# Kernel tuning notes

Hardware: AMD Instinct MI355X
Metric: run time of the kernel (lower is better)

Reference implementation:

```python
import jax, jax.numpy as jnp
import numpy as np

HEADS = 20
SHIFT = 0.6931471805599453  # style_alignment_score_shift = log(2)
KEY_SCALE = 1.0             # style_alignment_score_scale
EPS = 1e-5


def expand_first(feat, scale=1.0):
    # feat: [B, H, S, D]; broadcast style features (batch items 0 and B//2)
    b = feat.shape[0]
    fs = jnp.stack([feat[0], feat[b // 2]])[:, None]           # [2,1,H,S,D]
    fs = jnp.broadcast_to(fs, (2, b // 2) + feat.shape[1:])    # [2,B/2,H,S,D]
    if scale != 1:
        fs = jnp.concatenate([fs[:, :1], scale * fs[:, 1:]], axis=1)
    return fs.reshape(feat.shape)


def concat_first(feat, scale=1.0):
    # concatenate style features along the sequence axis (-2)
    return jnp.concatenate([feat, expand_first(feat, scale=scale)], axis=-2)


def adain(feat):
    # stats over sequence axis (-2); torch .var() is unbiased (ddof=1)
    mean = feat.mean(axis=-2, keepdims=True)
    std = jnp.sqrt(feat.var(axis=-2, keepdims=True, ddof=1) + EPS)
    sm = expand_first(mean)
    ss = expand_first(std)
    return (feat - mean) / std * ss + sm


def setup_inputs() -> dict:
    key = jax.random.key(0)
    ks = jax.random.split(key, 6)
    B, S, C = 4, 1024, 1280
    sc = 1.0 / np.sqrt(C)
    return {
        "hidden_states": jax.random.normal(ks[0], (B, S, C), jnp.float32),
        "Wq": jax.random.normal(ks[1], (C, C), jnp.float32) * sc,
        "Wk": jax.random.normal(ks[2], (C, C), jnp.float32) * sc,
        "Wv": jax.random.normal(ks[3], (C, C), jnp.float32) * sc,
        "Wo": jax.random.normal(ks[4], (C, C), jnp.float32) * sc,
        "bo": jnp.zeros((C,), jnp.float32),
    }


def reference(hidden_states, Wq, Wk, Wv, Wo, bo):
    B, S, C = hidden_states.shape
    H = HEADS
    hd = C // H
    scale = hd ** -0.5

    def to_heads(t):  # [B,S,C] -> [B,H,S,hd]
        return t.reshape(B, S, H, hd).transpose(0, 2, 1, 3)

    q = to_heads(hidden_states @ Wq.T)
    k = to_heads(hidden_states @ Wk.T)
    v = to_heads(hidden_states @ Wv.T)

    q = adain(q)              # adain_queries
    k = adain(k)              # adain_keys
    # adain_values = False

    k = concat_first(k, scale=KEY_SCALE)   # [B,H,2S,hd]
    v = concat_first(v)                    # [B,H,2S,hd]

    # shifted scaled dot-product attention (shift added to shared-key block)
    logits = jnp.einsum('bhqd,bhkd->bhqk', q, k) * scale  # [B,H,S,2S]
    bias = jnp.where(jnp.arange(k.shape[-2]) >= S, jnp.float32(SHIFT), jnp.float32(0.0))
    probs = jax.nn.softmax(logits + bias, axis=-1)
    out = jnp.einsum('bhqk,bhkd->bhqd', probs, v)         # [B,H,S,hd]

    out = out.transpose(0, 2, 1, 3).reshape(B, S, C)
    out = out @ Wo.T + bo
    return out
```

## Files before the change

### kernel.cpp

```cpp
#include <hip/hip_runtime.h>
#include <math.h>


typedef __bf16 bf16x8 __attribute__((ext_vector_type(8)));
typedef __bf16 bf16x2_t __attribute__((ext_vector_type(2)));
typedef float f32x4 __attribute__((ext_vector_type(4)));
typedef unsigned short u16x8 __attribute__((ext_vector_type(8)));

#define BDIM 256

__device__ inline unsigned short f2bf(float f) {
  return __builtin_bit_cast(unsigned short, (__bf16)f);
}
__device__ inline unsigned int pack_bf2(float lo, float hi) {
  bf16x2_t v;
  v[0] = (__bf16)lo;
  v[1] = (__bf16)hi;
  return __builtin_bit_cast(unsigned int, v);
}
__device__ inline float bf2f(unsigned short h) {
  return __uint_as_float(((unsigned int)h) << 16);
}

__device__ inline void gl_lds16(const unsigned short* g, unsigned short* l) {
  __builtin_amdgcn_global_load_lds(
      (const __attribute__((address_space(1))) unsigned int*)g,
      (__attribute__((address_space(3))) unsigned int*)l, 16, 0, 0);
}

__global__ __launch_bounds__(BDIM) void k_convert_all(
    const float* __restrict__ X, const float* __restrict__ Wq,
    const float* __restrict__ Wk, const float* __restrict__ Wv,
    const float* __restrict__ Wo, unsigned short* __restrict__ Xbf,
    unsigned short* __restrict__ Wcat, unsigned short* __restrict__ Wobf) {
  const int idx = blockIdx.x * BDIM + threadIdx.x;
  const float* src;
  unsigned short* dst;
  int off;
  if (idx < 1310720) {
    src = X; dst = Xbf; off = idx;
  } else {
    const int r = idx - 1310720;
    const int which = r / 409600;
    off = r - which * 409600;
    src = (which == 0) ? Wq : (which == 1) ? Wk : (which == 2) ? Wv : Wo;
    dst = (which < 3) ? Wcat + (size_t)which * 1638400 : Wobf;
  }
  const float4 v = ((const float4*)src)[off];
  ushort4 o;
  o.x = f2bf(v.x); o.y = f2bf(v.y); o.z = f2bf(v.z); o.w = f2bf(v.w);
  ((ushort4*)dst)[off] = o;
}

__global__ __launch_bounds__(512, 1) void k_gemm_bf16(
    const unsigned short* __restrict__ A, const unsigned short* __restrict__ B,
    unsigned short* __restrict__ Cbf, int M, int N, int K) {
  __shared__ unsigned short lds[2][2][16384];

  const int bid = blockIdx.x;
  const int swz = (bid & 7) * 30 + (bid >> 3);
  const int mt = swz & 15, nt = swz >> 4;
  const int mBase = mt * 256, nBase = nt * 256;

  const int t = threadIdx.x;
  const int w = t >> 6, lane = t & 63, quad = lane >> 4, l16 = lane & 15;
  const int wrow = w & 1, wcol = w >> 1;
  const int glg = (lane & 7) ^ ((lane >> 3) & 7);
  const int NTILES = K >> 6;

  f32x4 acc[8][4];
#pragma unroll
  for (int i = 0; i < 8; ++i)
#pragma unroll
    for (int j = 0; j < 4; ++j) acc[i][j] = (f32x4){0.f, 0.f, 0.f, 0.f};

  auto stage = [&](int s, int kt) {
#pragma unroll
    for (int j = 0; j < 4; ++j) {
      const int row = j * 64 + w * 8 + (lane >> 3);
      gl_lds16(A + (size_t)(mBase + row) * K + kt * 64 + glg * 8,
               &lds[s][0][(j * 512 + w * 64 + lane) * 8]);
    }
#pragma unroll
    for (int j = 0; j < 4; ++j) {
      const int row = j * 64 + w * 8 + (lane >> 3);
      gl_lds16(B + (size_t)(nBase + row) * K + kt * 64 + glg * 8,
               &lds[s][1][(j * 512 + w * 64 + lane) * 8]);
    }
  };

  stage(0, 0);
  stage(1, 1);
  asm volatile("s_waitcnt vmcnt(8)" ::: "memory");
  __builtin_amdgcn_s_barrier();

  const int arow0 = (wrow * 128 + l16) * 64;
  const int brow0 = (wcol * 64 + l16) * 64;
  const int g0 = ((quad) ^ (l16 & 7)) * 8;
  const int g1 = ((4 + quad) ^ (l16 & 7)) * 8;

  for (int kt = 0; kt < NTILES; ++kt) {
    const int s = kt & 1;
    if (kt >= 1 && kt + 1 < NTILES) stage(s ^ 1, kt + 1);
    const unsigned short* As = &lds[s][0][0];
    const unsigned short* Bs = &lds[s][1][0];
#pragma unroll
    for (int ph = 0; ph < 4; ++ph) {
      const int mh = ph >> 1, nh = ph & 1;
      bf16x8 af[4][2], bq[2][2];
#pragma unroll
      for (int mi = 0; mi < 4; ++mi) {
        const int ro = arow0 + (mh * 4 + mi) * 1024;
        af[mi][0] = *(const bf16x8*)(As + ro + g0);
        af[mi][1] = *(const bf16x8*)(As + ro + g1);
      }
#pragma unroll
      for (int ni = 0; ni < 2; ++ni) {
        const int ro = brow0 + (nh * 2 + ni) * 1024;
        bq[ni][0] = *(const bf16x8*)(Bs + ro + g0);
        bq[ni][1] = *(const bf16x8*)(Bs + ro + g1);
      }
      __builtin_amdgcn_s_setprio(1);
#pragma unroll
      for (int kk = 0; kk < 2; ++kk)
#pragma unroll
        for (int mi = 0; mi < 4; ++mi)
#pragma unroll
          for (int ni = 0; ni < 2; ++ni)
            acc[mh * 4 + mi][nh * 2 + ni] =
                __builtin_amdgcn_mfma_f32_16x16x32_bf16(
                    af[mi][kk], bq[ni][kk], acc[mh * 4 + mi][nh * 2 + ni], 0,
                    0, 0);
      __builtin_amdgcn_s_setprio(0);
      if (ph < 3) __builtin_amdgcn_s_barrier();
    }
    asm volatile("s_waitcnt vmcnt(0)" ::: "memory");
    __builtin_amdgcn_s_barrier();
  }

#pragma unroll
  for (int mi = 0; mi < 8; ++mi)
#pragma unroll
    for (int r = 0; r < 4; ++r) {
      const int row = mBase + wrow * 128 + mi * 16 + quad * 4 + r;
#pragma unroll
      for (int ni = 0; ni < 4; ++ni)
        Cbf[(size_t)row * N + nBase + wcol * 64 + ni * 16 + l16] =
            f2bf(acc[mi][ni][r]);
    }
}

__global__ __launch_bounds__(BDIM, 2) void k_gemm_out(
    const unsigned short* __restrict__ A, const unsigned short* __restrict__ B,
    float* __restrict__ Cf, const float* __restrict__ bias, int M, int N,
    int K) {
  __shared__ unsigned short lds[2][2][8192];

  const int bid = blockIdx.x;
  const int swz = (bid & 7) * 40 + (bid >> 3);
  const int mt = swz & 31, nt = swz >> 5;
  const int mBase = mt * 128, nBase = nt * 128;

  const int t = threadIdx.x;
  const int w = t >> 6, lane = t & 63, quad = lane >> 4, l16 = lane & 15;
  const int wrow = w & 1, wcol = w >> 1;
  const int glg = (lane & 7) ^ ((lane >> 3) & 7);
  const int NTILES = K >> 6;

  f32x4 acc[4][4];
#pragma unroll
  for (int i = 0; i < 4; ++i)
#pragma unroll
    for (int j = 0; j < 4; ++j) acc[i][j] = (f32x4){0.f, 0.f, 0.f, 0.f};

  auto stage = [&](int s, int kt) {
#pragma unroll
    for (int j = 0; j < 4; ++j) {
      const int row = j * 32 + (t >> 3);
      gl_lds16(A + (size_t)(mBase + row) * K + kt * 64 + glg * 8,
               &lds[s][0][(j * 256 + t) * 8]);
    }
#pragma unroll
    for (int j = 0; j < 4; ++j) {
      const int row = j * 32 + (t >> 3);
      gl_lds16(B + (size_t)(nBase + row) * K + kt * 64 + glg * 8,
               &lds[s][1][(j * 256 + t) * 8]);
    }
  };

  stage(0, 0);
  stage(1, 1);
  asm volatile("s_waitcnt vmcnt(8)" ::: "memory");
  __builtin_amdgcn_s_barrier();

  const int arow0 = (wrow * 64 + l16) * 64;
  const int brow0 = (wcol * 64 + l16) * 64;
  const int g0 = ((quad) ^ (l16 & 7)) * 8;
  const int g1 = ((4 + quad) ^ (l16 & 7)) * 8;

  for (int kt = 0; kt < NTILES; ++kt) {
    const int s = kt & 1;
    if (kt >= 1 && kt + 1 < NTILES) stage(s ^ 1, kt + 1);
    const unsigned short* As = &lds[s][0][0];
    const unsigned short* Bs = &lds[s][1][0];
#pragma unroll
    for (int ph = 0; ph < 2; ++ph) {
      bf16x8 af[2][2], bq[4][2];
#pragma unroll
      for (int mi = 0; mi < 2; ++mi) {
        const int ro = arow0 + (ph * 2 + mi) * 1024;
        af[mi][0] = *(const bf16x8*)(As + ro + g0);
        af[mi][1] = *(const bf16x8*)(As + ro + g1);
      }
#pragma unroll
      for (int ni = 0; ni < 4; ++ni) {
        const int ro = brow0 + ni * 1024;
        bq[ni][0] = *(const bf16x8*)(Bs + ro + g0);
        bq[ni][1] = *(const bf16x8*)(Bs + ro + g1);
      }
      __builtin_amdgcn_s_setprio(1);
#pragma unroll
      for (int kk = 0; kk < 2; ++kk)
#pragma unroll
        for (int mi = 0; mi < 2; ++mi)
#pragma unroll
          for (int ni = 0; ni < 4; ++ni)
            acc[ph * 2 + mi][ni] = __builtin_amdgcn_mfma_f32_16x16x32_bf16(
                af[mi][kk], bq[ni][kk], acc[ph * 2 + mi][ni], 0, 0, 0);
      __builtin_amdgcn_s_setprio(0);
      if (ph == 0) __builtin_amdgcn_s_barrier();
    }
    asm volatile("s_waitcnt vmcnt(0)" ::: "memory");
    __builtin_amdgcn_s_barrier();
  }

#pragma unroll
  for (int mi = 0; mi < 4; ++mi)
#pragma unroll
    for (int r = 0; r < 4; ++r) {
      const int row = mBase + wrow * 64 + mi * 16 + quad * 4 + r;
#pragma unroll
      for (int ni = 0; ni < 4; ++ni) {
        const int col = nBase + wcol * 64 + ni * 16 + l16;
        Cf[(size_t)row * N + col] = acc[mi][ni][r] + bias[col];
      }
    }
}

__global__ __launch_bounds__(320) void k_stats1(
    const unsigned short* __restrict__ QKV, float* __restrict__ psum,
    float* __restrict__ psq) {
  const int z = blockIdx.y, which = z >> 2, b = z & 3;
  const int c = threadIdx.x * 4;
  const size_t base =
      (size_t)(b * 1024 + blockIdx.x * 32) * 3840 + which * 1280 + c;
  float4 s = {0.f, 0.f, 0.f, 0.f}, s2 = {0.f, 0.f, 0.f, 0.f};
#pragma unroll 8
  for (int i = 0; i < 32; ++i) {
    const ushort4 xv = *(const ushort4*)(QKV + base + (size_t)i * 3840);
    const float x0 = bf2f(xv.x), x1 = bf2f(xv.y), x2 = bf2f(xv.z),
                x3 = bf2f(xv.w);
    s.x += x0; s.y += x1; s.z += x2; s.w += x3;
    s2.x = fmaf(x0, x0, s2.x); s2.y = fmaf(x1, x1, s2.y);
    s2.z = fmaf(x2, x2, s2.z); s2.w = fmaf(x3, x3, s2.w);
  }
  const size_t o = ((size_t)z * 32 + blockIdx.x) * 1280 + c;
  *(float4*)(psum + o) = s;
  *(float4*)(psq + o) = s2;
}

__global__ __launch_bounds__(BDIM) void k_stats2(
    const float* __restrict__ psum, const float* __restrict__ psq,
    float* __restrict__ stats) {
  const int z = blockIdx.y, which = z >> 2, b = z & 3;
  const int c = blockIdx.x * 256 + threadIdx.x;
  float s = 0.f, s2 = 0.f;
#pragma unroll
  for (int j = 0; j < 32; ++j) {
    s += psum[((size_t)z * 32 + j) * 1280 + c];
    s2 += psq[((size_t)z * 32 + j) * 1280 + c];
  }
  const float mean = s * (1.0f / 1024.0f);
  const float var = (s2 - 1024.0f * mean * mean) * (1.0f / 1023.0f);
  stats[((which * 2 + 0) * 4 + b) * 1280 + c] = mean;
  stats[((which * 2 + 1) * 4 + b) * 1280 + c] = sqrtf(var + 1e-5f);
}

__global__ __launch_bounds__(BDIM) void k_adain_vt(
    const unsigned short* __restrict__ QKV, const float* __restrict__ stats,
    unsigned short* __restrict__ qn, unsigned short* __restrict__ kn,
    unsigned short* __restrict__ vt) {
  __shared__ unsigned short tile[64][65];
  const int bx = blockIdx.x;
  if (bx < 10240) {
    const int which = bx / 5120;
    const int rem = bx - which * 5120;
    const int b = rem / 1280;
    const int xb = rem - b * 1280;
    const int idx = xb * BDIM + threadIdx.x;
    const int s = idx / 320;
    const int c = (idx - s * 320) * 4;
    const int sb = (b < 2) ? 0 : 2;
    const ushort4 xv = *(const ushort4*)(QKV + ((size_t)(b * 1024 + s)) * 3840 +
                                         which * 1280 + c);
    const float4 mean =
        *(const float4*)(stats + ((which * 2 + 0) * 4 + b) * 1280 + c);
    const float4 stdv =
        *(const float4*)(stats + ((which * 2 + 1) * 4 + b) * 1280 + c);
    const float4 meanS =
        *(const float4*)(stats + ((which * 2 + 0) * 4 + sb) * 1280 + c);
    const float4 stdS =
        *(const float4*)(stats + ((which * 2 + 1) * 4 + sb) * 1280 + c);
    ushort4 o;
    o.x = f2bf((bf2f(xv.x) - mean.x) / stdv.x * stdS.x + meanS.x);
    o.y = f2bf((bf2f(xv.y) - mean.y) / stdv.y * stdS.y + meanS.y);
    o.z = f2bf((bf2f(xv.z) - mean.z) / stdv.z * stdS.z + meanS.z);
    o.w = f2bf((bf2f(xv.w) - mean.w) / stdv.w * stdS.w + meanS.w);
    unsigned short* dst = (which == 0) ? qn : kn;
    *(ushort4*)(dst + ((size_t)(b * 1024 + s)) * 1280 + c) = o;
  } else {
    const int tb = bx - 10240;
    const int b = tb / 320;
    const int r2 = tb - b * 320;
    const int c0 = (r2 / 16) * 64;
    const int s0 = (r2 & 15) * 64;
    const int t = threadIdx.x;
    const int r = t >> 2, seg = (t & 3) * 16;
    const size_t goff = ((size_t)(b * 1024 + s0 + r)) * 3840 + 2560 + c0 + seg;
    const u16x8 va = *(const u16x8*)(QKV + goff);
    const u16x8 vb = *(const u16x8*)(QKV + goff + 8);
#pragma unroll
    for (int j = 0; j < 8; j++) {
      tile[r][seg + j] = va[j];
      tile[r][seg + 8 + j] = vb[j];
    }
    __syncthreads();
    u16x8 o0, o1;
#pragma unroll
    for (int j = 0; j < 8; j++) {
      o0[j] = tile[seg + j][r];
      o1[j] = tile[seg + 8 + j][r];
    }
    const size_t ooff = ((size_t)(b * 1280 + c0 + r)) * 1024 + s0 + seg;
    *(u16x8*)(vt + ooff) = o0;
    *(u16x8*)(vt + ooff + 8) = o1;
  }
}

__global__ __launch_bounds__(BDIM, 4) void k_attn(
    const unsigned short* __restrict__ qn, const unsigned short* __restrict__ kn,
    const unsigned short* __restrict__ vt, unsigned short* __restrict__ Opart,
    float* __restrict__ Lpart) {
  const int S = 1024, C = 1280;
  const int L = blockIdx.x + 8 * (blockIdx.y + 20 * blockIdx.z);
  const int qt = (L >> 3) & 7;
  const int hz = (L & 7) + ((L >> 6) << 3);
  const int h = hz % 20;
  const int zs = hz / 20;
  int b, chunk;
  if (zs < 2)      { b = 0; chunk = zs; }
  else if (zs < 6) { b = 1; chunk = zs - 2; }
  else if (zs < 8) { b = 2; chunk = zs - 6; }
  else             { b = 3; chunk = zs - 8; }
  const int ktBeg = chunk * 8;
  const int t = threadIdx.x, w = t >> 6, lane = t & 63;
  const int quad = lane >> 4, l16 = lane & 15;
  const int bstyle = (b < 2) ? 0 : 2;
  const int qrow = qt * 128 + w * 32;

  __shared__ unsigned short Ks[2][2][64 * 32];
  __shared__ unsigned short Vs[2][64 * 32];
  __shared__ unsigned short Plds[4][32][64];

  bf16x8 aq[2][2];
#pragma unroll
  for (int g = 0; g < 2; ++g) {
    const size_t qoff =
        ((size_t)(b * S + qrow + g * 16 + l16)) * C + h * 64 + quad * 8;
    aq[g][0] = *(const bf16x8*)(qn + qoff);
    aq[g][1] = *(const bf16x8*)(qn + qoff + 32);
  }

  bf16x8 ones;
#pragma unroll
  for (int i = 0; i < 8; ++i) ones[i] = (__bf16)1.0f;

  f32x4 o[2][4], lsum[2];
#pragma unroll
  for (int g = 0; g < 2; ++g) {
    lsum[g] = (f32x4){0.f, 0.f, 0.f, 0.f};
#pragma unroll
    for (int i = 0; i < 4; i++) o[g][i] = (f32x4){0.f, 0.f, 0.f, 0.f};
  }

  const int krow = t >> 2;
  const int kseg = ((t & 3) ^ ((t >> 3) & 3)) * 8;
  const int sw = l16 & 14;
  const int qsw = (quad ^ ((l16 >> 1) & 3)) * 8;

  auto stageK = [&](int buf, int kt) {
    const int bs = (kt < 16) ? b : bstyle;
    const int sk = (kt & 15) * 64;
    const unsigned short* kg =
        kn + (size_t)(bs * S + sk + krow) * C + h * 64 + kseg;
    gl_lds16(kg, Ks[buf][0] + t * 8);
    gl_lds16(kg + 32, Ks[buf][1] + t * 8);
  };
  auto stageV = [&](int kt) {
    const int bs = (kt < 16) ? b : bstyle;
    const int sk = (kt & 15) * 64;
    const unsigned short* vg =
        vt + (size_t)(bs * C + h * 64 + krow) * S + sk + kseg;
    gl_lds16(vg, Vs[0] + t * 8);
    gl_lds16(vg + 32, Vs[1] + t * 8);
  };

  stageK(0, ktBeg);

  const float SCALE2 = 0.125f * 1.44269504088896341f;

  for (int i = 0; i < 8; ++i) {
    const int kt = ktBeg + i;
    const int buf = i & 1;
    asm volatile("s_waitcnt vmcnt(0)" ::: "memory");
    __builtin_amdgcn_s_barrier();
    stageV(kt);
    if (i + 1 < 8) stageK(buf ^ 1, kt + 1);

    const float bias2 = (kt >= 16) ? 1.0f : 0.0f;

    f32x4 z2[2][4];
#pragma unroll
    for (int nt = 0; nt < 4; ++nt) {
      const bf16x8 bk0 =
          *(const bf16x8*)(Ks[buf][0] + (nt * 16 + l16) * 32 + qsw);
      const bf16x8 bk1 =
          *(const bf16x8*)(Ks[buf][1] + (nt * 16 + l16) * 32 + qsw);
#pragma unroll
      for (int g = 0; g < 2; ++g) {
        f32x4 zz = (f32x4){0.f, 0.f, 0.f, 0.f};
        zz = __builtin_amdgcn_mfma_f32_16x16x32_bf16(bk0, aq[g][0], zz, 0, 0, 0);
        zz = __builtin_amdgcn_mfma_f32_16x16x32_bf16(bk1, aq[g][1], zz, 0, 0, 0);
        z2[g][nt] = zz;
      }
    }

#pragma unroll
    for (int g = 0; g < 2; ++g) {
#pragma unroll
      for (int nt = 0; nt < 4; ++nt) {
        const float e0 = exp2f(fmaf(z2[g][nt][0], SCALE2, bias2));
        const float e1 = exp2f(fmaf(z2[g][nt][1], SCALE2, bias2));
        const float e2 = exp2f(fmaf(z2[g][nt][2], SCALE2, bias2));
        const float e3 = exp2f(fmaf(z2[g][nt][3], SCALE2, bias2));
        uint2 pk;
        pk.x = pack_bf2(e0, e1);
        pk.y = pack_bf2(e2, e3);
        const int phys = (nt * 4 + quad) ^ sw;
        *(uint2*)(&Plds[w][g * 16 + l16][phys * 4]) = pk;
      }
    }

    if (i + 1 < 8)
      asm volatile("s_waitcnt vmcnt(2)" ::: "memory");
    else
      asm volatile("s_waitcnt vmcnt(0)" ::: "memory");
    __builtin_amdgcn_s_barrier();

#pragma unroll
    for (int g = 0; g < 2; ++g) {
      const int a0 = (2 * quad) ^ sw;
      const int a1 = (2 * quad + 8) ^ sw;
      const bf16x8 pa0 = *(const bf16x8*)(&Plds[w][g * 16 + l16][a0 * 4]);
      const bf16x8 pa1 = *(const bf16x8*)(&Plds[w][g * 16 + l16][a1 * 4]);
      lsum[g] = __builtin_amdgcn_mfma_f32_16x16x32_bf16(pa0, ones, lsum[g], 0, 0, 0);
      lsum[g] = __builtin_amdgcn_mfma_f32_16x16x32_bf16(pa1, ones, lsum[g], 0, 0, 0);
#pragma unroll
      for (int dt = 0; dt < 4; ++dt) {
        const bf16x8 vb0 =
            *(const bf16x8*)(Vs[0] + (dt * 16 + l16) * 32 + qsw);
        const bf16x8 vb1 =
            *(const bf16x8*)(Vs[1] + (dt * 16 + l16) * 32 + qsw);
        o[g][dt] =
            __builtin_amdgcn_mfma_f32_16x16x32_bf16(pa0, vb0, o[g][dt], 0, 0, 0);
        o[g][dt] =
            __builtin_amdgcn_mfma_f32_16x16x32_bf16(pa1, vb1, o[g][dt], 0, 0, 0);
      }
    }
  }

  if (l16 == 0) {
#pragma unroll
    for (int g = 0; g < 2; ++g)
#pragma unroll
      for (int r = 0; r < 4; ++r)
        Lpart[((size_t)zs * 20 + h) * 1024 + qrow + g * 16 + quad * 4 + r] =
            lsum[g][r];
  }

  unsigned short* Op = Opart + (size_t)zs * 1024 * 1280;
#pragma unroll
  for (int g = 0; g < 2; ++g)
#pragma unroll
    for (int dt = 0; dt < 4; ++dt)
#pragma unroll
      for (int r = 0; r < 4; ++r)
        Op[(size_t)(qrow + g * 16 + quad * 4 + r) * 1280 + h * 64 + dt * 16 +
           l16] = f2bf(o[g][dt][r]);
}

__global__ __launch_bounds__(BDIM) void k_combine(
    const unsigned short* __restrict__ Opart, const float* __restrict__ Lpart,
    unsigned short* __restrict__ attnb) {
  const int idx = blockIdx.x * BDIM + threadIdx.x;
  const int row = idx / 160;
  const int c = (idx - row * 160) * 8;
  const int b = row >> 10, q = row & 1023, h = c >> 6;
  const int zb = (b >> 1) * 6 + (b & 1) * 2;
  const int ns = 2 + (b & 1) * 2;
  float L = 0.f;
  float acc[8] = {0.f, 0.f, 0.f, 0.f, 0.f, 0.f, 0.f, 0.f};
  for (int s = 0; s < ns; ++s) {
    L += Lpart[((size_t)(zb + s) * 20 + h) * 1024 + q];
    const u16x8 v =
        *(const u16x8*)(Opart + (size_t)(zb + s) * 1310720 + (size_t)q * 1280 + c);
#pragma unroll
    for (int j = 0; j < 8; ++j) acc[j] += bf2f(v[j]);
  }
  const float rl = 1.0f / L;
  u16x8 o8;
#pragma unroll
  for (int j = 0; j < 8; ++j) o8[j] = f2bf(acc[j] * rl);
  *(u16x8*)(attnb + (size_t)row * 1280 + c) = o8;
}

extern "C" void kernel_launch(void* const* d_in, const int* in_sizes, int n_in,
                              void* d_out, int out_size, void* d_ws,
                              size_t ws_size, hipStream_t stream) {
  const float* X = (const float*)d_in[0];
  const float* Wq = (const float*)d_in[1];
  const float* Wk = (const float*)d_in[2];
  const float* Wv = (const float*)d_in[3];
  const float* Wo = (const float*)d_in[4];
  const float* bo = (const float*)d_in[5];
  float* out = (float*)d_out;

  char* ws = (char*)d_ws;
  size_t off = 0;
  auto alloc = [&](size_t bytes) {
    char* p = ws + off;
    off += (bytes + 255) & ~(size_t)255;
    return p;
  };
  unsigned short* Wcat = (unsigned short*)alloc(3840ull * 1280 * 2);
  unsigned short* Xbf = (unsigned short*)alloc(4096ull * 1280 * 2);
  unsigned short* QKV = (unsigned short*)alloc(4096ull * 3840 * 2);
  unsigned short* Wobf = (unsigned short*)alloc(1280ull * 1280 * 2);
  float* stats = (float*)alloc(2ull * 2 * 4 * 1280 * 4);
  unsigned short* qnb = (unsigned short*)alloc(4096ull * 1280 * 2);
  unsigned short* knb = (unsigned short*)alloc(4096ull * 1280 * 2);
  unsigned short* vtb = (unsigned short*)alloc(4096ull * 1280 * 2);
  unsigned short* attnb = (unsigned short*)alloc(4096ull * 1280 * 2);

  unsigned short* Opart = QKV;
  float* Lpart = (float*)Wcat;
  float* psum = (float*)attnb;
  float* psq = (float*)(attnb + 4096ull * 1280 / 2);

  k_convert_all<<<11520, BDIM, 0, stream>>>(X, Wq, Wk, Wv, Wo, Xbf, Wcat, Wobf);
  k_gemm_bf16<<<240, 512, 0, stream>>>(Xbf, Wcat, QKV, 4096, 3840, 1280);
  k_stats1<<<dim3(32, 8), 320, 0, stream>>>(QKV, psum, psq);
  k_stats2<<<dim3(5, 8), BDIM, 0, stream>>>(psum, psq, stats);
  k_adain_vt<<<11520, BDIM, 0, stream>>>(QKV, stats, qnb, knb, vtb);
  k_attn<<<dim3(8, 20, 12), BDIM, 0, stream>>>(qnb, knb, vtb, Opart, Lpart);
  k_combine<<<2560, BDIM, 0, stream>>>(Opart, Lpart, attnb);
  k_gemm_out<<<320, BDIM, 0, stream>>>(attnb, Wobf, out, bo, 4096, 1280, 1280);
}
```

Baseline: 262.2 us.

## Fold key AdaIN into query scaling and per-row bias inside attention

The separate AdaIN pass over Q and K is removed. The attention kernel now normalizes Q in registers from raw QKV and reads un-normalized K directly. The key affine transform (gain and offset) is folded algebraically into the query: the gain multiplies the query, and the offset becomes a per-row additive bias reduced by wave shuffles. For style chunks the key stats are treated as identity, which relies on the style batch's keys mapping onto themselves. This saves a full read/write pass over Q and K, at the cost of extra per-block prologue math and the precision risk of rounding the scaled query to bf16. The partial-output buffers are remapped onto Xbf and qnb, because QKV is still being read during attention.

```diff
diff --git a/kernel.cpp b/kernel.cpp
--- a/kernel.cpp
+++ b/kernel.cpp
@@ -286,72 +286,41 @@
   stats[((which * 2 + 1) * 4 + b) * 1280 + c] = sqrtf(var + 1e-5f);
 }
 
-__global__ __launch_bounds__(BDIM) void k_adain_vt(
-    const unsigned short* __restrict__ QKV, const float* __restrict__ stats,
-    unsigned short* __restrict__ qn, unsigned short* __restrict__ kn,
-    unsigned short* __restrict__ vt) {
+__global__ __launch_bounds__(BDIM) void k_vt(
+    const unsigned short* __restrict__ QKV, unsigned short* __restrict__ vt) {
   __shared__ unsigned short tile[64][65];
-  const int bx = blockIdx.x;
-  if (bx < 10240) {
-    const int which = bx / 5120;
-    const int rem = bx - which * 5120;
-    const int b = rem / 1280;
-    const int xb = rem - b * 1280;
-    const int idx = xb * BDIM + threadIdx.x;
-    const int s = idx / 320;
-    const int c = (idx - s * 320) * 4;
-    const int sb = (b < 2) ? 0 : 2;
-    const ushort4 xv = *(const ushort4*)(QKV + ((size_t)(b * 1024 + s)) * 3840 +
-                                         which * 1280 + c);
-    const float4 mean =
-        *(const float4*)(stats + ((which * 2 + 0) * 4 + b) * 1280 + c);
-    const float4 stdv =
-        *(const float4*)(stats + ((which * 2 + 1) * 4 + b) * 1280 + c);
-    const float4 meanS =
-        *(const float4*)(stats + ((which * 2 + 0) * 4 + sb) * 1280 + c);
-    const float4 stdS =
-        *(const float4*)(stats + ((which * 2 + 1) * 4 + sb) * 1280 + c);
-    ushort4 o;
-    o.x = f2bf((bf2f(xv.x) - mean.x) / stdv.x * stdS.x + meanS.x);
-    o.y = f2bf((bf2f(xv.y) - mean.y) / stdv.y * stdS.y + meanS.y);
-    o.z = f2bf((bf2f(xv.z) - mean.z) / stdv.z * stdS.z + meanS.z);
-    o.w = f2bf((bf2f(xv.w) - mean.w) / stdv.w * stdS.w + meanS.w);
-    unsigned short* dst = (which == 0) ? qn : kn;
-    *(ushort4*)(dst + ((size_t)(b * 1024 + s)) * 1280 + c) = o;
-  } else {
-    const int tb = bx - 10240;
-    const int b = tb / 320;
-    const int r2 = tb - b * 320;
-    const int c0 = (r2 / 16) * 64;
-    const int s0 = (r2 & 15) * 64;
-    const int t = threadIdx.x;
-    const int r = t >> 2, seg = (t & 3) * 16;
-    const size_t goff = ((size_t)(b * 1024 + s0 + r)) * 3840 + 2560 + c0 + seg;
-    const u16x8 va = *(const u16x8*)(QKV + goff);
-    const u16x8 vb = *(const u16x8*)(QKV + goff + 8);
-#pragma unroll
-    for (int j = 0; j < 8; j++) {
-      tile[r][seg + j] = va[j];
-      tile[r][seg + 8 + j] = vb[j];
-    }
-    __syncthreads();
-    u16x8 o0, o1;
-#pragma unroll
-    for (int j = 0; j < 8; j++) {
-      o0[j] = tile[seg + j][r];
-      o1[j] = tile[seg + 8 + j][r];
-    }
-    const size_t ooff = ((size_t)(b * 1280 + c0 + r)) * 1024 + s0 + seg;
-    *(u16x8*)(vt + ooff) = o0;
-    *(u16x8*)(vt + ooff + 8) = o1;
-  }
+  const int tb = blockIdx.x;
+  const int b = tb / 320;
+  const int r2 = tb - b * 320;
+  const int c0 = (r2 / 16) * 64;
+  const int s0 = (r2 & 15) * 64;
+  const int t = threadIdx.x;
+  const int r = t >> 2, seg = (t & 3) * 16;
+  const size_t goff = ((size_t)(b * 1024 + s0 + r)) * 3840 + 2560 + c0 + seg;
+  const u16x8 va = *(const u16x8*)(QKV + goff);
+  const u16x8 vb = *(const u16x8*)(QKV + goff + 8);
+#pragma unroll
+  for (int j = 0; j < 8; j++) {
+    tile[r][seg + j] = va[j];
+    tile[r][seg + 8 + j] = vb[j];
+  }
+  __syncthreads();
+  u16x8 o0, o1;
+#pragma unroll
+  for (int j = 0; j < 8; j++) {
+    o0[j] = tile[seg + j][r];
+    o1[j] = tile[seg + 8 + j][r];
+  }
+  const size_t ooff = ((size_t)(b * 1280 + c0 + r)) * 1024 + s0 + seg;
+  *(u16x8*)(vt + ooff) = o0;
+  *(u16x8*)(vt + ooff + 8) = o1;
 }
 
 __global__ __launch_bounds__(BDIM, 4) void k_attn(
-    const unsigned short* __restrict__ qn, const unsigned short* __restrict__ kn,
-    const unsigned short* __restrict__ vt, unsigned short* __restrict__ Opart,
-    float* __restrict__ Lpart) {
-  const int S = 1024, C = 1280;
+    const unsigned short* __restrict__ qkv, const float* __restrict__ stats,
+    const unsigned short* __restrict__ vt, unsigned short* __restrict__ Op0,
+    unsigned short* __restrict__ Op1, float* __restrict__ Lpart) {
+  const int S = 1024;
   const int L = blockIdx.x + 8 * (blockIdx.y + 20 * blockIdx.z);
   const int qt = (L >> 3) & 7;
   const int hz = (L & 7) + ((L >> 6) << 3);
@@ -367,18 +336,76 @@
   const int quad = lane >> 4, l16 = lane & 15;
   const int bstyle = (b < 2) ? 0 : 2;
   const int qrow = qt * 128 + w * 32;
+  const bool style = (ktBeg >= 16);
 
   __shared__ unsigned short Ks[2][2][64 * 32];
   __shared__ unsigned short Vs[2][64 * 32];
   __shared__ unsigned short Plds[4][32][64];
 
+  const float S2 = 0.125f * 1.44269504088896341f;
+
   bf16x8 aq[2][2];
-#pragma unroll
-  for (int g = 0; g < 2; ++g) {
-    const size_t qoff =
-        ((size_t)(b * S + qrow + g * 16 + l16)) * C + h * 64 + quad * 8;
-    aq[g][0] = *(const bf16x8*)(qn + qoff);
-    aq[g][1] = *(const bf16x8*)(qn + qoff + 32);
+  float biasv[2];
+  {
+    float rq[2] = {0.f, 0.f};
+#pragma unroll
+    for (int hf = 0; hf < 2; ++hf) {
+      const int cc = h * 64 + quad * 8 + hf * 32;
+      float mqb[8], sqb[8], mqs[8], sqs[8];
+      *(float4*)(mqb)     = *(const float4*)(stats + (0 + b) * 1280 + cc);
+      *(float4*)(mqb + 4) = *(const float4*)(stats + (0 + b) * 1280 + cc + 4);
+      *(float4*)(sqb)     = *(const float4*)(stats + (4 + b) * 1280 + cc);
+      *(float4*)(sqb + 4) = *(const float4*)(stats + (4 + b) * 1280 + cc + 4);
+      *(float4*)(mqs)     = *(const float4*)(stats + (0 + bstyle) * 1280 + cc);
+      *(float4*)(mqs + 4) = *(const float4*)(stats + (0 + bstyle) * 1280 + cc + 4);
+      *(float4*)(sqs)     = *(const float4*)(stats + (4 + bstyle) * 1280 + cc);
+      *(float4*)(sqs + 4) = *(const float4*)(stats + (4 + bstyle) * 1280 + cc + 4);
+      float gk[8], ok[8];
+      if (!style) {
+        float mkb[8], skb[8], mks[8], sks[8];
+        *(float4*)(mkb)     = *(const float4*)(stats + (8 + b) * 1280 + cc);
+        *(float4*)(mkb + 4) = *(const float4*)(stats + (8 + b) * 1280 + cc + 4);
+        *(float4*)(skb)     = *(const float4*)(stats + (12 + b) * 1280 + cc);
+        *(float4*)(skb + 4) = *(const float4*)(stats + (12 + b) * 1280 + cc + 4);
+        *(float4*)(mks)     = *(const float4*)(stats + (8 + bstyle) * 1280 + cc);
+        *(float4*)(mks + 4) = *(const float4*)(stats + (8 + bstyle) * 1280 + cc + 4);
+        *(float4*)(sks)     = *(const float4*)(stats + (12 + bstyle) * 1280 + cc);
+        *(float4*)(sks + 4) = *(const float4*)(stats + (12 + bstyle) * 1280 + cc + 4);
+#pragma unroll
+        for (int j = 0; j < 8; ++j) {
+          gk[j] = sks[j] / skb[j];
+          ok[j] = mks[j] - mkb[j] * gk[j];
+        }
+      }
+#pragma unroll
+      for (int g = 0; g < 2; ++g) {
+        const size_t qoff =
+            ((size_t)(b * S + qrow + g * 16 + l16)) * 3840 + cc;
+        const bf16x8 qv = *(const bf16x8*)(qkv + qoff);
+        bf16x8 av;
+#pragma unroll
+        for (int j = 0; j < 8; ++j) {
+          const float q = (float)qv[j];
+          const float qn = (q - mqb[j]) / sqb[j] * sqs[j] + mqs[j];
+          float a;
+          if (!style) {
+            rq[g] = fmaf(qn, ok[j], rq[g]);
+            a = qn * gk[j] * S2;
+          } else {
+            a = qn * S2;
+          }
+          av[j] = (__bf16)a;
+        }
+        aq[g][hf] = av;
+      }
+    }
+#pragma unroll
+    for (int g = 0; g < 2; ++g) {
+      float r = rq[g] * S2;
+      r += __shfl_xor(r, 16, 64);
+      r += __shfl_xor(r, 32, 64);
+      biasv[g] = style ? 1.0f : r;
+    }
   }
 
   bf16x8 ones;
@@ -402,7 +429,7 @@
     const int bs = (kt < 16) ? b : bstyle;
     const int sk = (kt & 15) * 64;
     const unsigned short* kg =
-        kn + (size_t)(bs * S + sk + krow) * C + h * 64 + kseg;
+        qkv + (size_t)(bs * S + sk + krow) * 3840 + 1280 + h * 64 + kseg;
     gl_lds16(kg, Ks[buf][0] + t * 8);
     gl_lds16(kg + 32, Ks[buf][1] + t * 8);
   };
@@ -410,14 +437,12 @@
     const int bs = (kt < 16) ? b : bstyle;
     const int sk = (kt & 15) * 64;
     const unsigned short* vg =
-        vt + (size_t)(bs * C + h * 64 + krow) * S + sk + kseg;
+        vt + (size_t)(bs * 1280 + h * 64 + krow) * S + sk + kseg;
     gl_lds16(vg, Vs[0] + t * 8);
     gl_lds16(vg + 32, Vs[1] + t * 8);
   };
 
   stageK(0, ktBeg);
-
-  const float SCALE2 = 0.125f * 1.44269504088896341f;
 
   for (int i = 0; i < 8; ++i) {
     const int kt = ktBeg + i;
@@ -427,8 +452,6 @@
     stageV(kt);
     if (i + 1 < 8) stageK(buf ^ 1, kt + 1);
 
-    const float bias2 = (kt >= 16) ? 1.0f : 0.0f;
-
     f32x4 z2[2][4];
 #pragma unroll
     for (int nt = 0; nt < 4; ++nt) {
@@ -447,12 +470,13 @@
 
 #pragma unroll
     for (int g = 0; g < 2; ++g) {
+      const float bg = biasv[g];
 #pragma unroll
       for (int nt = 0; nt < 4; ++nt) {
-        const float e0 = exp2f(fmaf(z2[g][nt][0], SCALE2, bias2));
-        const float e1 = exp2f(fmaf(z2[g][nt][1], SCALE2, bias2));
-        const float e2 = exp2f(fmaf(z2[g][nt][2], SCALE2, bias2));
-        const float e3 = exp2f(fmaf(z2[g][nt][3], SCALE2, bias2));
+        const float e0 = exp2f(z2[g][nt][0] + bg);
+        const float e1 = exp2f(z2[g][nt][1] + bg);
+        const float e2 = exp2f(z2[g][nt][2] + bg);
+        const float e3 = exp2f(z2[g][nt][3] + bg);
         uint2 pk;
         pk.x = pack_bf2(e0, e1);
         pk.y = pack_bf2(e2, e3);
@@ -498,7 +522,8 @@
             lsum[g][r];
   }
 
-  unsigned short* Op = Opart + (size_t)zs * 1024 * 1280;
+  unsigned short* Op = (zs < 4) ? Op0 + (size_t)zs * 1310720
+                                : Op1 + (size_t)(zs - 4) * 1310720;
 #pragma unroll
   for (int g = 0; g < 2; ++g)
 #pragma unroll
@@ -510,8 +535,8 @@
 }
 
 __global__ __launch_bounds__(BDIM) void k_combine(
-    const unsigned short* __restrict__ Opart, const float* __restrict__ Lpart,
-    unsigned short* __restrict__ attnb) {
+    const unsigned short* __restrict__ Op0, const unsigned short* __restrict__ Op1,
+    const float* __restrict__ Lpart, unsigned short* __restrict__ attnb) {
   const int idx = blockIdx.x * BDIM + threadIdx.x;
   const int row = idx / 160;
   const int c = (idx - row * 160) * 8;
@@ -521,9 +546,12 @@
   float L = 0.f;
   float acc[8] = {0.f, 0.f, 0.f, 0.f, 0.f, 0.f, 0.f, 0.f};
   for (int s = 0; s < ns; ++s) {
-    L += Lpart[((size_t)(zb + s) * 20 + h) * 1024 + q];
-    const u16x8 v =
-        *(const u16x8*)(Opart + (size_t)(zb + s) * 1310720 + (size_t)q * 1280 + c);
+    const int z = zb + s;
+    const unsigned short* base = (z < 4)
+        ? Op0 + (size_t)z * 1310720
+        : Op1 + (size_t)(z - 4) * 1310720;
+    L += Lpart[((size_t)z * 20 + h) * 1024 + q];
+    const u16x8 v = *(const u16x8*)(base + (size_t)q * 1280 + c);
 #pragma unroll
     for (int j = 0; j < 8; ++j) acc[j] += bf2f(v[j]);
   }
@@ -561,8 +589,10 @@
   unsigned short* knb = (unsigned short*)alloc(4096ull * 1280 * 2);
   unsigned short* vtb = (unsigned short*)alloc(4096ull * 1280 * 2);
   unsigned short* attnb = (unsigned short*)alloc(4096ull * 1280 * 2);
-
-  unsigned short* Opart = QKV;
+  (void)knb;
+
+  unsigned short* Op0 = Xbf;
+  unsigned short* Op1 = qnb;
   float* Lpart = (float*)Wcat;
   float* psum = (float*)attnb;
   float* psq = (float*)(attnb + 4096ull * 1280 / 2);
@@ -571,8 +601,9 @@
   k_gemm_bf16<<<240, 512, 0, stream>>>(Xbf, Wcat, QKV, 4096, 3840, 1280);
   k_stats1<<<dim3(32, 8), 320, 0, stream>>>(QKV, psum, psq);
   k_stats2<<<dim3(5, 8), BDIM, 0, stream>>>(psum, psq, stats);
-  k_adain_vt<<<11520, BDIM, 0, stream>>>(QKV, stats, qnb, knb, vtb);
-  k_attn<<<dim3(8, 20, 12), BDIM, 0, stream>>>(qnb, knb, vtb, Opart, Lpart);
-  k_combine<<<2560, BDIM, 0, stream>>>(Opart, Lpart, attnb);
+  k_vt<<<1280, BDIM, 0, stream>>>(QKV, vtb);
+  k_attn<<<dim3(8, 20, 12), BDIM, 0, stream>>>(QKV, stats, vtb, Op0, Op1,
+                                               Lpart);
+  k_combine<<<2560, BDIM, 0, stream>>>(Op0, Op1, Lpart, attnb);
   k_gemm_out<<<320, BDIM, 0, stream>>>(attnb, Wobf, out, bo, 4096, 1280, 1280);
 }
```

Measured after the change: 265.4 us. Within noise of the previous version (+1.2%).
